# Kernel optimization log

Measured on AMD Instinct MI355X. Metric: run time of the kernel, lower is better.

The kernel has to match this reference:

```python
import jax, jax.numpy as jnp
from jax import lax
import numpy as np
import math

# --- static config (matches init_kwargs) ---
B, L, C_IN = 64, 1024, 16
D, H, D_FF = 256, 8, 1024
HS, E_LAYERS, OUT = 256, 2, 1
MA, FACTOR = 25, 3
TOP_K = int(FACTOR * math.log(L))  # 20


def _ln(x, g, b, eps=1e-5):
    m = x.mean(-1, keepdims=True)
    v = ((x - m) ** 2).mean(-1, keepdims=True)
    return (x - m) / jnp.sqrt(v + eps) * g + b


def _series_decomp(x, k):
    # x: [B, L, C]; replicate-pad then moving average (AvgPool1d stride 1)
    pad = (k - 1) // 2
    front = jnp.repeat(x[:, :1, :], pad, axis=1)
    end = jnp.repeat(x[:, -1:, :], pad, axis=1)
    xp = jnp.concatenate([front, x, end], axis=1)  # [B, L+k-1, C]
    cs = jnp.cumsum(xp, axis=1)
    cs = jnp.concatenate([jnp.zeros_like(cs[:, :1]), cs], axis=1)
    mm = (cs[:, k:] - cs[:, :-k]) / k  # [B, L, C]
    return x - mm, mm


def _autocorrelation(q, k, v):
    # q,k,v: [B, L, H, E] -> eval-mode Autoformer AutoCorrelation
    Bq, Lq, Hq, Eq = q.shape
    qf = jnp.fft.rfft(q.transpose(0, 2, 3, 1), axis=-1)  # [B,H,E,F]
    kf = jnp.fft.rfft(k.transpose(0, 2, 3, 1), axis=-1)
    corr = jnp.fft.irfft(qf * jnp.conj(kf), n=Lq, axis=-1)  # [B,H,E,L]
    mean_value = corr.mean(axis=(1, 2))  # [B, L]
    weights, delay = lax.top_k(mean_value, TOP_K)  # [B, K]
    tmp_corr = jax.nn.softmax(weights, axis=-1)
    vals = v.transpose(0, 2, 3, 1)  # [B,H,E,L]
    init = jnp.arange(Lq)

    def step(acc, dw):
        d, w = dw  # d: [B] int, w: [B] float
        idx = (init[None, :] + d[:, None]) % Lq  # circular delayed gather == roll
        pat = jnp.take_along_axis(vals, idx[:, None, None, :], axis=-1)
        return acc + pat * w[:, None, None, None], None

    agg, _ = lax.scan(step, jnp.zeros_like(vals), (delay.T, tmp_corr.T))
    return agg.transpose(0, 3, 1, 2)  # [B, L, H, E]


def _forward(x_enc, conv1_w, conv1_b, conv2_w, conv2_b, cnn_ln_g, cnn_ln_b,
             proj_w, proj_b, proj_ln_g, proj_ln_b,
             Wq, bq, Wk, bk, Wv, bv, Wo, bo, Wff1, Wff2,
             rp1_w, rp1_b, rp_ln_g, rp_ln_b, rp2_w, rp2_b):
    Bb = x_enc.shape[0]
    dn = ('NCH', 'OIH', 'NCH')
    # CNN frontend (dropout = identity in eval)
    h = lax.conv_general_dilated(x_enc.transpose(0, 2, 1), conv1_w, (1,), [(1, 1)],
                                 dimension_numbers=dn) + conv1_b[None, :, None]
    h = jax.nn.relu(h)
    h = lax.conv_general_dilated(h, conv2_w, (1,), [(1, 1)],
                                 dimension_numbers=dn) + conv2_b[None, :, None]
    h = jax.nn.relu(h)
    enc = _ln(h.transpose(0, 2, 1), cnn_ln_g, cnn_ln_b)  # [B, L, D]

    pooled_parts = []
    for i in range(E_LAYERS):
        q = (enc @ Wq[i] + bq[i]).reshape(Bb, L, H, D // H)
        k = (enc @ Wk[i] + bk[i]).reshape(Bb, L, H, D // H)
        v = (enc @ Wv[i] + bv[i]).reshape(Bb, L, H, D // H)
        ac = _autocorrelation(q, k, v).reshape(Bb, L, D)
        new_x = ac @ Wo[i] + bo[i]
        x = enc + new_x
        x, _ = _series_decomp(x, MA)
        y = jax.nn.gelu(jnp.einsum('bld,fd->blf', x, Wff1[i]), approximate=False)
        y = jnp.einsum('blf,df->bld', y, Wff2[i])
        enc, _ = _series_decomp(x + y, MA)
        pooled_parts.append(enc[:, -1, :])

    pooled = jnp.concatenate(pooled_parts, axis=-1)  # [B, e_layers*D]
    input_embed = _ln(jax.nn.relu(x_enc.reshape(Bb, -1) @ proj_w + proj_b),
                      proj_ln_g, proj_ln_b)  # [B, HS]
    final = jnp.concatenate([pooled, input_embed], axis=-1)
    o = jax.nn.relu(final @ rp1_w + rp1_b)
    o = _ln(o, rp_ln_g, rp_ln_b)
    o = o @ rp2_w + rp2_b  # [B, 1]
    return o.squeeze(-1)


def setup_inputs() -> dict:
    key = jax.random.key(0)
    ks = iter(jax.random.split(key, 32))

    def nrm(shape, s=0.02):
        return jax.random.normal(next(ks), shape, jnp.float32) * s

    inp = {
        'x_enc': jax.random.normal(next(ks), (B, L, C_IN), jnp.float32),
        'conv1_w': nrm((D, C_IN, 3), 0.1), 'conv1_b': jnp.zeros((D,), jnp.float32),
        'conv2_w': nrm((D, D, 3), 0.05), 'conv2_b': jnp.zeros((D,), jnp.float32),
        'cnn_ln_g': jnp.ones((D,), jnp.float32), 'cnn_ln_b': jnp.zeros((D,), jnp.float32),
        'proj_w': nrm((L * C_IN, HS)), 'proj_b': jnp.zeros((HS,), jnp.float32),
        'proj_ln_g': jnp.ones((HS,), jnp.float32), 'proj_ln_b': jnp.zeros((HS,), jnp.float32),
        'Wq': nrm((E_LAYERS, D, D)), 'bq': jnp.zeros((E_LAYERS, D), jnp.float32),
        'Wk': nrm((E_LAYERS, D, D)), 'bk': jnp.zeros((E_LAYERS, D), jnp.float32),
        'Wv': nrm((E_LAYERS, D, D)), 'bv': jnp.zeros((E_LAYERS, D), jnp.float32),
        'Wo': nrm((E_LAYERS, D, D)), 'bo': jnp.zeros((E_LAYERS, D), jnp.float32),
        'Wff1': nrm((E_LAYERS, D_FF, D)),
        'Wff2': nrm((E_LAYERS, D, D_FF)),
        'rp1_w': nrm((E_LAYERS * D + HS, HS)), 'rp1_b': jnp.zeros((HS,), jnp.float32),
        'rp_ln_g': jnp.ones((HS,), jnp.float32), 'rp_ln_b': jnp.zeros((HS,), jnp.float32),
        'rp2_w': nrm((HS, OUT)), 'rp2_b': jnp.zeros((OUT,), jnp.float32),
    }
    return inp


def reference(x_enc, conv1_w, conv1_b, conv2_w, conv2_b, cnn_ln_g, cnn_ln_b,
              proj_w, proj_b, proj_ln_g, proj_ln_b,
              Wq, bq, Wk, bk, Wv, bv, Wo, bo, Wff1, Wff2,
              rp1_w, rp1_b, rp_ln_g, rp_ln_b, rp2_w, rp2_b):
    return _forward(x_enc, conv1_w, conv1_b, conv2_w, conv2_b, cnn_ln_g, cnn_ln_b,
                    proj_w, proj_b, proj_ln_g, proj_ln_b,
                    Wq, bq, Wk, bk, Wv, bv, Wo, bo, Wff1, Wff2,
                    rp1_w, rp1_b, rp_ln_g, rp_ln_b, rp2_w, rp2_b)
```

## Files before the change

### kernel.cpp

```cpp
#include <hip/hip_runtime.h>
#include <math.h>

#define FLAG_ACC     1
#define FLAG_RELU    2
#define FLAG_GELU    4
#define FLAG_ABF16   8
#define FLAG_OBF16  16
#define FLAG_RESB16 32

typedef __attribute__((ext_vector_type(8))) short short8;
typedef __attribute__((ext_vector_type(4))) short short4v;
typedef __attribute__((ext_vector_type(4))) float f32x4;

__device__ __forceinline__ short f2bf(float f) {
  unsigned u = __builtin_bit_cast(unsigned, f);
  unsigned r = u + 0x7fffu + ((u >> 16) & 1u);
  return (short)(r >> 16);
}
__device__ __forceinline__ float bf2f(short s) {
  unsigned u = ((unsigned)(unsigned short)s) << 16;
  return __builtin_bit_cast(float, u);
}
__device__ __forceinline__ void load_lds16(const void* g, void* lds) {
  __builtin_amdgcn_global_load_lds(
      (const __attribute__((address_space(1))) void*)g,
      (__attribute__((address_space(3))) void*)lds, 16, 0, 0);
}

__global__ __launch_bounds__(256) void gemm_f32(
    const float* __restrict__ A, const float* __restrict__ B, float* __restrict__ C,
    int M, int N, int K, int a_shift,
    const float* __restrict__ bias, const float* __restrict__ residual, int flags)
{
  __shared__ float As[16][65];
  __shared__ float Bs[16][64];
  const int tid = threadIdx.x;
  const int tx = tid & 15, ty = tid >> 4;
  const int row0 = blockIdx.y * 64;
  const int col0 = blockIdx.x * 64;
  int kbeg = 0, kend = K;
  if ((int)gridDim.z > 1) {
    int kchunk = ((K + (int)gridDim.z - 1) / (int)gridDim.z + 15) & ~15;
    kbeg = (int)blockIdx.z * kchunk;
    kend = min(K, kbeg + kchunk);
  }
  float acc[4][4] = {};
  const int a_m = tid >> 2;
  const int a_k = (tid & 3) << 2;
  const int b_n = (tid & 15) << 2;
  const int b_k = tid >> 4;
  for (int k0 = kbeg; k0 < kend; k0 += 16) {
    int srow = row0 + a_m + a_shift;
    float4 av = make_float4(0.f, 0.f, 0.f, 0.f);
    if (srow >= 0 && srow < M)
      av = *reinterpret_cast<const float4*>(A + (long long)srow * K + (k0 + a_k));
    As[a_k + 0][a_m] = av.x; As[a_k + 1][a_m] = av.y;
    As[a_k + 2][a_m] = av.z; As[a_k + 3][a_m] = av.w;
    float4 bv = make_float4(0.f, 0.f, 0.f, 0.f);
    int brow = k0 + b_k;
    if (brow < K)
      bv = *reinterpret_cast<const float4*>(B + (long long)brow * N + (col0 + b_n));
    Bs[b_k][b_n + 0] = bv.x; Bs[b_k][b_n + 1] = bv.y;
    Bs[b_k][b_n + 2] = bv.z; Bs[b_k][b_n + 3] = bv.w;
    __syncthreads();
#pragma unroll
    for (int kk = 0; kk < 16; kk++) {
      float ar[4], br[4];
#pragma unroll
      for (int i = 0; i < 4; i++) ar[i] = As[kk][ty * 4 + i];
#pragma unroll
      for (int j = 0; j < 4; j++) br[j] = Bs[kk][tx * 4 + j];
#pragma unroll
      for (int i = 0; i < 4; i++)
#pragma unroll
        for (int j = 0; j < 4; j++)
          acc[i][j] += ar[i] * br[j];
    }
    __syncthreads();
  }
  if ((int)gridDim.z > 1) {
#pragma unroll
    for (int i = 0; i < 4; i++) {
      int r = row0 + ty * 4 + i; if (r >= M) continue;
#pragma unroll
      for (int j = 0; j < 4; j++) {
        int c = col0 + tx * 4 + j; if (c >= N) continue;
        atomicAdd(&C[(long long)r * N + c], acc[i][j]);
      }
    }
    return;
  }
#pragma unroll
  for (int i = 0; i < 4; i++) {
    int r = row0 + ty * 4 + i; if (r >= M) continue;
#pragma unroll
    for (int j = 0; j < 4; j++) {
      int c = col0 + tx * 4 + j; if (c >= N) continue;
      float v = acc[i][j];
      if (bias)     v += bias[c];
      if (residual) v += residual[(long long)r * N + c];
      if (flags & FLAG_ACC)  v += C[(long long)r * N + c];
      if (flags & FLAG_RELU) v = fmaxf(v, 0.f);
      if (flags & FLAG_GELU) v = 0.5f * v * (1.f + erff(v * 0.70710678118654752f));
      C[(long long)r * N + c] = v;
    }
  }
}

__global__ __launch_bounds__(256) void gemm_bf16_bt(
    const void* __restrict__ Av, const short* __restrict__ Btb, void* __restrict__ Cv,
    const float* __restrict__ residual, const float* __restrict__ bias,
    int M, int N, int K, int lda, int flags, int tapped)
{
  __shared__ __align__(16) short Asl[2][8192];
  __shared__ __align__(16) short Bsl[2][8192];
  const int tid = threadIdx.x;
  const int row0 = blockIdx.x * 128;
  const int col0 = blockIdx.y * 128;
  const int lane = tid & 63;
  const int wave = tid >> 6;
  const int wm = (wave >> 1) * 64;
  const int wn = (wave & 1) * 64;
  const int fm = lane & 15;
  const int k8c = lane >> 4;
  const int mr = tid >> 1;
  const int mkc = (tid & 1) * 4;
  const int msw = mr & 7;
  const bool a_dma = (flags & FLAG_ABF16) && !tapped;

  short8 sv[4];

  auto stage_dma = [&](int buf, int k0) {
#pragma unroll
    for (int u = 0; u < 4; u++) {
      int p = (wave * 4 + u) * 64 + lane;
      int r = p >> 3;
      int kc = (p & 7) ^ (r & 7);
      load_lds16(Btb + (long long)(col0 + r) * K + k0 + kc * 8,
                 (char*)Bsl[buf] + (wave * 4 + u) * 1024);
      if (a_dma)
        load_lds16((const short*)Av + (long long)(row0 + r) * lda + k0 + kc * 8,
                   (char*)Asl[buf] + (wave * 4 + u) * 1024);
    }
  };
  auto loadA = [&](int k0) {
    int arow = row0 + mr + (tapped ? (k0 >> 8) - 1 : 0);
    int acol = tapped ? (k0 & 255) : k0;
    bool ok = (arow >= 0 && arow < M);
    if (flags & FLAG_ABF16) {
      const short* ga = (const short*)Av + (long long)arow * lda + acol + mkc * 8;
      short8 z;
#pragma unroll
      for (int u = 0; u < 8; u++) z[u] = 0;
#pragma unroll
      for (int j = 0; j < 4; j++) sv[j] = ok ? *(const short8*)(ga + j * 8) : z;
    } else {
      const float* ga = (const float*)Av + (long long)arow * lda + acol + mkc * 8;
#pragma unroll
      for (int j = 0; j < 4; j++) {
        float4 f0 = make_float4(0.f,0.f,0.f,0.f), f1 = f0;
        if (ok) { f0 = *(const float4*)(ga + j * 8); f1 = *(const float4*)(ga + j * 8 + 4); }
        short8 v;
        v[0]=f2bf(f0.x); v[1]=f2bf(f0.y); v[2]=f2bf(f0.z); v[3]=f2bf(f0.w);
        v[4]=f2bf(f1.x); v[5]=f2bf(f1.y); v[6]=f2bf(f1.z); v[7]=f2bf(f1.w);
        sv[j] = v;
      }
    }
  };
  auto writeA = [&](int buf) {
#pragma unroll
    for (int j = 0; j < 4; j++)
      *(short8*)&Asl[buf][(mr * 8 + ((mkc + j) ^ msw)) * 8] = sv[j];
  };

  f32x4 acc[4][4] = {};
  const int nt = K >> 6;
  stage_dma(0, 0);
  if (!a_dma) { loadA(0); writeA(0); }
  __syncthreads();
  int cur = 0;
  for (int t = 0; t < nt; t++) {
    if (t + 1 < nt) {
      stage_dma(cur ^ 1, (t + 1) << 6);
      if (!a_dma) loadA((t + 1) << 6);
    }
#pragma unroll
    for (int kk8 = 0; kk8 < 8; kk8 += 4) {
      short8 af[4], bf[4];
#pragma unroll
      for (int i = 0; i < 4; i++) {
        int r = wm + i * 16 + fm;
        af[i] = *(short8*)&Asl[cur][(r * 8 + ((kk8 + k8c) ^ (r & 7))) * 8];
      }
#pragma unroll
      for (int j = 0; j < 4; j++) {
        int r = wn + j * 16 + fm;
        bf[j] = *(short8*)&Bsl[cur][(r * 8 + ((kk8 + k8c) ^ (r & 7))) * 8];
      }
#pragma unroll
      for (int i = 0; i < 4; i++)
#pragma unroll
        for (int j = 0; j < 4; j++)
          acc[i][j] = __builtin_amdgcn_mfma_f32_16x16x32_bf16(af[i], bf[j], acc[i][j], 0, 0, 0);
    }
    if (!a_dma && t + 1 < nt) writeA(cur ^ 1);
    __syncthreads();
    cur ^= 1;
  }
#pragma unroll
  for (int i = 0; i < 4; i++) {
    const int mbase = row0 + wm + i * 16 + (lane >> 4) * 4;
#pragma unroll
    for (int j = 0; j < 4; j++) {
      const int n = col0 + wn + j * 16 + fm;
      const float bs = bias ? bias[n] : 0.f;
#pragma unroll
      for (int r = 0; r < 4; r++) {
        long long idx = (long long)(mbase + r) * N + n;
        float v = acc[i][j][r] + bs;
        if (residual) {
          if (flags & FLAG_RESB16) v += bf2f(((const short*)residual)[idx]);
          else                     v += residual[idx];
        }
        if (flags & FLAG_ACC)  v += ((const float*)Cv)[idx];
        if (flags & FLAG_RELU) v = fmaxf(v, 0.f);
        if (flags & FLAG_GELU) v = 0.5f * v * (1.f + erff(v * 0.70710678118654752f));
        if (flags & FLAG_OBF16) ((short*)Cv)[idx] = f2bf(v);
        else                    ((float*)Cv)[idx] = v;
      }
    }
  }
}

__global__ __launch_bounds__(256) void gemm_qkT(
    const short* __restrict__ Ab, const short* __restrict__ Bth,
    const short* __restrict__ Btl, float* __restrict__ QT,
    const float* __restrict__ bias, int K)
{
  __shared__ __align__(16) short Asl[2][4096];
  __shared__ __align__(16) short Bhi[2][4096];
  __shared__ __align__(16) short Blo[2][4096];
  const int tid = threadIdx.x;
  const int row0 = blockIdx.x * 128;
  const int col0 = blockIdx.y * 128;
  const int lane = tid & 63;
  const int wave = tid >> 6;
  const int wm = (wave >> 1) * 64;
  const int wn = (wave & 1) * 64;
  const int fm = lane & 15;
  const int k8c = lane >> 4;

  auto stage = [&](int buf, int k0) {
#pragma unroll
    for (int u = 0; u < 2; u++) {
      int p = (wave + u * 4) * 64 + lane;
      int r = p >> 2;
      int kc = (p & 3) ^ ((r >> 1) & 3);
      long long ao = (long long)(row0 + r) * 256 + k0 + kc * 8;
      long long go = (long long)(col0 + r) * K + k0 + kc * 8;
      int lo = (wave + u * 4) * 1024;
      load_lds16(Ab + ao, (char*)Asl[buf] + lo);
      load_lds16(Bth + go, (char*)Bhi[buf] + lo);
      load_lds16(Btl + go, (char*)Blo[buf] + lo);
    }
  };

  f32x4 acc[4][4] = {};
  const int nt = K >> 5;
  stage(0, 0);
  __syncthreads();
  int cur = 0;
  for (int t = 0; t < nt; t++) {
    if (t + 1 < nt) stage(cur ^ 1, (t + 1) << 5);
    short8 af[4], bh[4], bl[4];
#pragma unroll
    for (int i = 0; i < 4; i++) {
      int r = wm + i * 16 + fm;
      af[i] = *(short8*)&Asl[cur][(r * 4 + (k8c ^ ((r >> 1) & 3))) * 8];
    }
#pragma unroll
    for (int j = 0; j < 4; j++) {
      int r = wn + j * 16 + fm;
      int p = (r * 4 + (k8c ^ ((r >> 1) & 3))) * 8;
      bh[j] = *(short8*)&Bhi[cur][p];
      bl[j] = *(short8*)&Blo[cur][p];
    }
#pragma unroll
    for (int i = 0; i < 4; i++)
#pragma unroll
      for (int j = 0; j < 4; j++) {
        acc[i][j] = __builtin_amdgcn_mfma_f32_16x16x32_bf16(af[i], bh[j], acc[i][j], 0, 0, 0);
        acc[i][j] = __builtin_amdgcn_mfma_f32_16x16x32_bf16(af[i], bl[j], acc[i][j], 0, 0, 0);
      }
    __syncthreads();
    cur ^= 1;
  }
#pragma unroll
  for (int i = 0; i < 4; i++) {
    const int mbase = row0 + wm + i * 16 + (lane >> 4) * 4;
    const int bb = mbase >> 10;
    const int l  = mbase & 1023;
#pragma unroll
    for (int j = 0; j < 4; j++) {
      const int n = col0 + wn + j * 16 + fm;
      const float bs = bias[n];
      float4 o = make_float4(acc[i][j][0] + bs, acc[i][j][1] + bs,
                             acc[i][j][2] + bs, acc[i][j][3] + bs);
      *(float4*)&QT[((long long)(bb * 512 + n) << 10) + l] = o;
    }
  }
}

#define SKW(i) ((i) + ((i) >> 5))

__device__ __forceinline__ int rev4_10(int f) {
  return ((f & 3) << 8) | (((f >> 2) & 3) << 6) | (((f >> 4) & 3) << 4)
       | (((f >> 6) & 3) << 2) | ((f >> 8) & 3);
}

template<int M, bool INV, int NCH>
__device__ __forceinline__ void fft_stageN(float2 (*__restrict__ buf)[1056],
                                           const float2* __restrict__ tw, int t) {
  constexpr int LOG2M = (M == 256) ? 8 : (M == 64) ? 6 : (M == 16) ? 4 : (M == 4) ? 2 : 0;
  const int j = t & (M - 1);
  const int base = ((t >> LOG2M) << (LOG2M + 2)) | j;
  float2 w = tw[SKW(j << (8 - LOG2M))];
  const float c1 = w.x, s1 = INV ? -w.y : w.y;
  const float c2 = c1 * c1 - s1 * s1, s2 = 2.f * c1 * s1;
  const float c3 = c2 * c1 - s2 * s1, s3 = c2 * s1 + s2 * c1;
#pragma unroll
  for (int ch = 0; ch < NCH; ch++) {
    float2* s = buf[ch];
    float2 a0 = s[SKW(base)];
    float2 b0 = s[SKW(base + M)];
    float2 d0 = s[SKW(base + 2 * M)];
    float2 e0 = s[SKW(base + 3 * M)];
    float t0r = a0.x + d0.x, t0i = a0.y + d0.y;
    float t1r = a0.x - d0.x, t1i = a0.y - d0.y;
    float t2r = b0.x + e0.x, t2i = b0.y + e0.y;
    float t3r = b0.x - e0.x, t3i = b0.y - e0.y;
    float y0r = t0r + t2r, y0i = t0i + t2i;
    float y2r = t0r - t2r, y2i = t0i - t2i;
    float y1r, y1i, y3r, y3i;
    if (!INV) { y1r = t1r + t3i; y1i = t1i - t3r; y3r = t1r - t3i; y3i = t1i + t3r; }
    else      { y1r = t1r - t3i; y1i = t1i + t3r; y3r = t1r + t3i; y3i = t1i - t3r; }
    s[SKW(base)]         = make_float2(y0r, y0i);
    s[SKW(base + M)]     = make_float2(y1r * c1 - y1i * s1, y1r * s1 + y1i * c1);
    s[SKW(base + 2 * M)] = make_float2(y2r * c2 - y2i * s2, y2r * s2 + y2i * c2);
    s[SKW(base + 3 * M)] = make_float2(y3r * c3 - y3i * s3, y3r * s3 + y3i * c3);
  }
}

__global__ __launch_bounds__(256) void fft_cross(
    const float* __restrict__ QT, float* __restrict__ Rpart)
{
  __shared__ float2 buf[4][1056];
  __shared__ float2 tw[264];
  const int tid = threadIdx.x;
  const int b = blockIdx.x & 63;
  const int g = blockIdx.x >> 6;
  {
    float s, c;
    sincosf(-1.5707963267948966f * (float)tid * (1.f / 256.f), &s, &c);
    tw[SKW(tid)] = make_float2(c, s);
  }
  const float* Qb = QT + (long long)b * 524288;
  const int c0 = g * 16;
  float4 qv[4], kv[4];
#pragma unroll
  for (int c = 0; c < 4; c++) {
    qv[c] = *(const float4*)(Qb + ((long long)(c0 + c) << 10) + tid * 4);
    kv[c] = *(const float4*)(Qb + ((long long)(256 + c0 + c) << 10) + tid * 4);
  }
  float aR[4] = {0.f, 0.f, 0.f, 0.f}, aI[4] = {0.f, 0.f, 0.f, 0.f};
  __syncthreads();
  for (int q4 = 0; q4 < 4; q4++) {
    const int i0 = tid * 4;
#pragma unroll
    for (int c = 0; c < 4; c++) {
      buf[c][SKW(i0 + 0)] = make_float2(qv[c].x, kv[c].x);
      buf[c][SKW(i0 + 1)] = make_float2(qv[c].y, kv[c].y);
      buf[c][SKW(i0 + 2)] = make_float2(qv[c].z, kv[c].z);
      buf[c][SKW(i0 + 3)] = make_float2(qv[c].w, kv[c].w);
    }
    if (q4 < 3) {
      const int cb = c0 + (q4 + 1) * 4;
#pragma unroll
      for (int c = 0; c < 4; c++) {
        qv[c] = *(const float4*)(Qb + ((long long)(cb + c) << 10) + tid * 4);
        kv[c] = *(const float4*)(Qb + ((long long)(256 + cb + c) << 10) + tid * 4);
      }
    }
    __syncthreads();
    fft_stageN<256, false, 4>(buf, tw, tid); __syncthreads();
    fft_stageN<64,  false, 4>(buf, tw, tid); __syncthreads();
    fft_stageN<16,  false, 4>(buf, tw, tid); __syncthreads();
    fft_stageN<4,   false, 4>(buf, tw, tid); __syncthreads();
    fft_stageN<1,   false, 4>(buf, tw, tid); __syncthreads();
#pragma unroll
    for (int u = 0; u < 4; u++) {
      const int f = tid + (u << 8);
      const int p1 = SKW(rev4_10(f));
      const int p2 = SKW(rev4_10((1024 - f) & 1023));
#pragma unroll
      for (int c = 0; c < 4; c++) {
        float2 z1 = buf[c][p1];
        float2 z2 = buf[c][p2];
        float Qr = 0.5f * (z1.x + z2.x), Qi = 0.5f * (z1.y - z2.y);
        float Kr = 0.5f * (z1.y + z2.y), Ki = 0.5f * (z2.x - z1.x);
        aR[u] += Qr * Kr + Qi * Ki;
        aI[u] += Qi * Kr - Qr * Ki;
      }
    }
    __syncthreads();
  }
  float* Rp = Rpart + (long long)(g * 64 + b) * 2048;
#pragma unroll
  for (int u = 0; u < 4; u++) {
    Rp[tid + (u << 8)] = aR[u];
    Rp[1024 + tid + (u << 8)] = aI[u];
  }
}

__global__ __launch_bounds__(256) void fft_inv(
    const float* __restrict__ Rpart, float* __restrict__ MV)
{
  __shared__ float2 ping[1056], tw[264];
  const int tid = threadIdx.x;
  const int b = blockIdx.x;
  {
    float s, c;
    sincosf(-1.5707963267948966f * (float)tid * (1.f / 256.f), &s, &c);
    tw[SKW(tid)] = make_float2(c, s);
  }
#pragma unroll
  for (int u = 0; u < 4; u++) {
    int f = tid + (u << 8);
    float sr = 0.f, si = 0.f;
#pragma unroll
    for (int g = 0; g < 16; g++) {
      const float* Rp = Rpart + (long long)(g * 64 + b) * 2048;
      sr += Rp[f];
      si += Rp[1024 + f];
    }
    ping[SKW(f)] = make_float2(sr, si);
  }
  __syncthreads();
  float2 (*bp)[1056] = reinterpret_cast<float2 (*)[1056]>(ping);
  fft_stageN<256, true, 1>(bp, tw, tid); __syncthreads();
  fft_stageN<64,  true, 1>(bp, tw, tid); __syncthreads();
  fft_stageN<16,  true, 1>(bp, tw, tid); __syncthreads();
  fft_stageN<4,   true, 1>(bp, tw, tid); __syncthreads();
  fft_stageN<1,   true, 1>(bp, tw, tid); __syncthreads();
  const float sc = 1.f / (1024.f * 256.f);
#pragma unroll
  for (int u = 0; u < 4; u++) {
    int p = tid + (u << 8);
    MV[(long long)b * 1024 + rev4_10(p)] = ping[SKW(p)].x * sc;
  }
}

__global__ void prep_weights(
    const float* __restrict__ conv2_w, const float* __restrict__ Wq,
    const float* __restrict__ Wk, const float* __restrict__ Wff1,
    const float* __restrict__ Wff2,
    const float* __restrict__ bq, const float* __restrict__ bk,
    short* __restrict__ CB2Tb, short* __restrict__ QKTH, short* __restrict__ QKTL,
    short* __restrict__ WFF1b, short* __restrict__ WFF2b, float* __restrict__ BQK)
{
  const int total = 196608 + 262144 + 524288 + 524288 + 1024;
  for (int idx = blockIdx.x * 256 + threadIdx.x; idx < total;
       idx += gridDim.x * 256) {
    int t = idx;
    if (t < 196608) {
      int o = t / 768, rem = t % 768, kk = rem >> 8, i = rem & 255;
      CB2Tb[t] = f2bf(conv2_w[(o * 256 + i) * 3 + kk]);
    } else if ((t -= 196608) < 262144) {
      int L = t >> 17, rem = t & 131071, r = rem >> 8, k = rem & 255;
      float val = (r < 256) ? Wq[L * 65536 + k * 256 + r]
                            : Wk[L * 65536 + k * 256 + (r - 256)];
      short h = f2bf(val);
      QKTH[t] = h;
      QKTL[t] = f2bf(val - bf2f(h));
    } else if ((t -= 262144) < 524288) {
      WFF1b[t] = f2bf(Wff1[t]);
    } else if ((t -= 524288) < 524288) {
      WFF2b[t] = f2bf(Wff2[t]);
    } else {
      t -= 524288;
      int L = t >> 9, j = t & 511;
      BQK[t] = (j < 256) ? bq[L * 256 + j] : bk[L * 256 + (j - 256)];
    }
  }
}

__global__ void vo_finish(const float* __restrict__ WVO, const float* __restrict__ Wo,
                          const float* __restrict__ bv, const float* __restrict__ bo,
                          short* __restrict__ WVOTb, float* __restrict__ BVO)
{
  const int total = 131072 + 512;
  for (int idx = blockIdx.x * 256 + threadIdx.x; idx < total;
       idx += gridDim.x * 256) {
    if (idx < 131072) {
      int L = idx >> 16, rem = idx & 65535, n = rem >> 8, k = rem & 255;
      WVOTb[idx] = f2bf(WVO[L * 65536 + k * 256 + n]);
    } else {
      int j = idx - 131072;
      int L = j >> 8, n = j & 255;
      float acc = bo[L * 256 + n];
      for (int k = 0; k < 256; k++)
        acc += bv[L * 256 + k] * Wo[(long long)L * 65536 + k * 256 + n];
      BVO[j] = acc;
    }
  }
}

__global__ __launch_bounds__(256) void conv1_direct(
    const float* __restrict__ x, const float* __restrict__ w,
    const float* __restrict__ bias, short* __restrict__ out)
{
  __shared__ float xs[66][16];
  const int b = blockIdx.y, lg = blockIdx.x, tid = threadIdx.x;
  const int l0 = lg * 64;
  for (int idx = tid; idx < 1056; idx += 256) {
    int r = idx >> 4, c = idx & 15;
    int l = l0 + r - 1;
    xs[r][c] = (l >= 0 && l < 1024) ? x[((long long)b * 1024 + l) * 16 + c] : 0.f;
  }
  float wr[48];
#pragma unroll
  for (int u = 0; u < 48; u++) wr[u] = w[tid * 48 + u];
  const float bs = bias[tid];
  __syncthreads();
  for (int r = 0; r < 64; r++) {
    float acc = bs;
#pragma unroll
    for (int i = 0; i < 16; i++) {
      acc += xs[r + 0][i] * wr[i * 3 + 0];
      acc += xs[r + 1][i] * wr[i * 3 + 1];
      acc += xs[r + 2][i] * wr[i * 3 + 2];
    }
    out[((long long)b * 1024 + l0 + r) * 256 + tid] = f2bf(fmaxf(acc, 0.f));
  }
}

__global__ void fixup_conv_b(short* __restrict__ h, const short* __restrict__ src,
                             const float* __restrict__ w, const float* __restrict__ bias)
{
  int b = blockIdx.x >> 1;
  int l = (blockIdx.x & 1) ? 1023 : 0;
  int o = threadIdx.x;
  float acc = bias[o];
  for (int kk = 0; kk < 3; kk++) {
    int t = l + kk - 1;
    if (t < 0 || t > 1023) continue;
    const short* srow = src + ((long long)b * 1024 + t) * 256;
    const float* wrow = w + (long long)o * 256 * 3 + kk;
    for (int i = 0; i < 256; i++) acc += bf2f(srow[i]) * wrow[(long long)i * 3];
  }
  h[((long long)b * 1024 + l) * 256 + o] = f2bf(fmaxf(acc, 0.f));
}

__global__ __launch_bounds__(256) void ln_rows4(
    const float* __restrict__ in, float* __restrict__ out,
    const float* __restrict__ g, const float* __restrict__ b,
    int prerelu, int out_stride, int out_off)
{
  const int row = blockIdx.x * 4 + (threadIdx.x >> 6);
  const int lane = threadIdx.x & 63;
  float4 x = ((const float4*)(in + (long long)row * 256))[lane];
  if (prerelu) {
    x.x = fmaxf(x.x, 0.f); x.y = fmaxf(x.y, 0.f);
    x.z = fmaxf(x.z, 0.f); x.w = fmaxf(x.w, 0.f);
  }
  float s = x.x + x.y + x.z + x.w;
#pragma unroll
  for (int o = 32; o > 0; o >>= 1) s += __shfl_xor(s, o, 64);
  float mean = s * (1.f / 256.f);
  float4 d = make_float4(x.x - mean, x.y - mean, x.z - mean, x.w - mean);
  float s2 = d.x * d.x + d.y * d.y + d.z * d.z + d.w * d.w;
#pragma unroll
  for (int o = 32; o > 0; o >>= 1) s2 += __shfl_xor(s2, o, 64);
  float rsd = rsqrtf(s2 * (1.f / 256.f) + 1e-5f);
  float4 gg = ((const float4*)g)[lane];
  float4 bb = ((const float4*)b)[lane];
  float4 o4 = make_float4(d.x * rsd * gg.x + bb.x, d.y * rsd * gg.y + bb.y,
                          d.z * rsd * gg.z + bb.z, d.w * rsd * gg.w + bb.w);
  ((float4*)(out + (long long)row * out_stride + out_off))[lane] = o4;
}

__global__ __launch_bounds__(256) void ln_rows4bb(
    const short* __restrict__ in, short* __restrict__ out,
    const float* __restrict__ g, const float* __restrict__ b)
{
  const int row = blockIdx.x * 4 + (threadIdx.x >> 6);
  const int lane = threadIdx.x & 63;
  short4v xb = ((const short4v*)in)[(long long)row * 64 + lane];
  float4 x = make_float4(bf2f(xb[0]), bf2f(xb[1]), bf2f(xb[2]), bf2f(xb[3]));
  float s = x.x + x.y + x.z + x.w;
#pragma unroll
  for (int o = 32; o > 0; o >>= 1) s += __shfl_xor(s, o, 64);
  float mean = s * (1.f / 256.f);
  float4 d = make_float4(x.x - mean, x.y - mean, x.z - mean, x.w - mean);
  float s2 = d.x * d.x + d.y * d.y + d.z * d.z + d.w * d.w;
#pragma unroll
  for (int o = 32; o > 0; o >>= 1) s2 += __shfl_xor(s2, o, 64);
  float rsd = rsqrtf(s2 * (1.f / 256.f) + 1e-5f);
  float4 gg = ((const float4*)g)[lane];
  float4 bb = ((const float4*)b)[lane];
  short4v o4;
  o4[0] = f2bf(d.x * rsd * gg.x + bb.x);
  o4[1] = f2bf(d.y * rsd * gg.y + bb.y);
  o4[2] = f2bf(d.z * rsd * gg.z + bb.z);
  o4[3] = f2bf(d.w * rsd * gg.w + bb.w);
  ((short4v*)out)[(long long)row * 64 + lane] = o4;
}

__global__ void decomp4bf(const short* __restrict__ in, short* __restrict__ out,
                          float* __restrict__ fin, int finoff)
{
  const int id = blockIdx.x;
  const int c = id & 7;
  const int s = id >> 3;
  const int b = c + 8 * (s >> 8);
  const int lg = s & 255;
  const int l = lg * 4 + (threadIdx.x >> 6);
  const int c4 = threadIdx.x & 63;
  const short4v* base = (const short4v*)(in + (long long)b * 262144);
  float4 acc = make_float4(0.f, 0.f, 0.f, 0.f);
#pragma unroll
  for (int j = -12; j <= 12; j++) {
    int t = l + j;
    t = t < 0 ? 0 : (t > 1023 ? 1023 : t);
    short4v x = base[t * 64 + c4];
    acc.x += bf2f(x[0]); acc.y += bf2f(x[1]);
    acc.z += bf2f(x[2]); acc.w += bf2f(x[3]);
  }
  short4v x0 = base[l * 64 + c4];
  float4 o = make_float4(bf2f(x0[0]) - acc.x * (1.f / 25.f),
                         bf2f(x0[1]) - acc.y * (1.f / 25.f),
                         bf2f(x0[2]) - acc.z * (1.f / 25.f),
                         bf2f(x0[3]) - acc.w * (1.f / 25.f));
  short4v ob;
  ob[0] = f2bf(o.x); ob[1] = f2bf(o.y); ob[2] = f2bf(o.z); ob[3] = f2bf(o.w);
  ((short4v*)out)[((long long)b * 1024 + l) * 64 + c4] = ob;
  if (l == 1023) {
    float* f = fin + (long long)b * 768 + finoff + c4 * 4;
    f[0] = o.x; f[1] = o.y; f[2] = o.z; f[3] = o.w;
  }
}

__global__ void decomp4b(const short* __restrict__ in, short* __restrict__ out)
{
  const int id = blockIdx.x;
  const int c = id & 7;
  const int s = id >> 3;
  const int b = c + 8 * (s >> 8);
  const int lg = s & 255;
  const int l = lg * 4 + (threadIdx.x >> 6);
  const int c4 = threadIdx.x & 63;
  const short4v* base = (const short4v*)(in + (long long)b * 262144);
  float4 acc = make_float4(0.f, 0.f, 0.f, 0.f);
#pragma unroll
  for (int j = -12; j <= 12; j++) {
    int t = l + j;
    t = t < 0 ? 0 : (t > 1023 ? 1023 : t);
    short4v x = base[t * 64 + c4];
    acc.x += bf2f(x[0]); acc.y += bf2f(x[1]);
    acc.z += bf2f(x[2]); acc.w += bf2f(x[3]);
  }
  short4v x0 = base[l * 64 + c4];
  short4v o;
  o[0] = f2bf(bf2f(x0[0]) - acc.x * (1.f / 25.f));
  o[1] = f2bf(bf2f(x0[1]) - acc.y * (1.f / 25.f));
  o[2] = f2bf(bf2f(x0[2]) - acc.z * (1.f / 25.f));
  o[3] = f2bf(bf2f(x0[3]) - acc.w * (1.f / 25.f));
  ((short4v*)(out + (long long)b * 262144))[l * 64 + c4] = o;
}

__global__ __launch_bounds__(64) void topk_softmax_wave(
    const float* __restrict__ mv, float* __restrict__ wts, int* __restrict__ dly)
{
  const int b = blockIdx.x, lane = threadIdx.x;
  float v[16];
#pragma unroll
  for (int j = 0; j < 16; j++)
    v[j] = mv[(long long)b * 1024 + lane + 64 * j];
  float selv = 0.f; int seli = 0;
  for (int it = 0; it < 20; it++) {
    float bv = -1e30f; int bi = 0x7fffffff;
#pragma unroll
    for (int j = 0; j < 16; j++) {
      float x = v[j]; int idx = lane + 64 * j;
      if (x > bv || (x == bv && idx < bi)) { bv = x; bi = idx; }
    }
#pragma unroll
    for (int off = 32; off > 0; off >>= 1) {
      float ov = __shfl_xor(bv, off, 64);
      int   oi = __shfl_xor(bi, off, 64);
      if (ov > bv || (ov == bv && oi < bi)) { bv = ov; bi = oi; }
    }
    if (lane == it) { selv = bv; seli = bi; }
    if ((bi & 63) == lane) v[bi >> 6] = -1e30f;
  }
  const float w0 = __shfl(selv, 0, 64);
  float e = (lane < 20) ? __expf(selv - w0) : 0.f;
  float s = e;
#pragma unroll
  for (int off = 32; off > 0; off >>= 1) s += __shfl_xor(s, off, 64);
  if (lane < 20) {
    wts[b * 20 + lane] = e / s;
    dly[b * 20 + lane] = seli;
  }
}

__global__ void agg4b(const short* __restrict__ enc, const float* __restrict__ wts,
                      const int* __restrict__ dly, short* __restrict__ out)
{
  const int id = blockIdx.x;
  const int c = id & 7;
  const int s = id >> 3;
  const int b = c + 8 * (s >> 8);
  const int lg = s & 255;
  const int l = lg * 4 + (threadIdx.x >> 6);
  const int c4 = threadIdx.x & 63;
  const short4v* vb = (const short4v*)(enc + (long long)b * 262144);
  float4 acc = make_float4(0.f, 0.f, 0.f, 0.f);
  for (int kk = 0; kk < 20; kk++) {
    int d = dly[b * 20 + kk];
    float w = wts[b * 20 + kk];
    short4v x = vb[((l + d) & 1023) * 64 + c4];
    acc.x += w * bf2f(x[0]); acc.y += w * bf2f(x[1]);
    acc.z += w * bf2f(x[2]); acc.w += w * bf2f(x[3]);
  }
  short4v o;
  o[0] = f2bf(acc.x); o[1] = f2bf(acc.y); o[2] = f2bf(acc.z); o[3] = f2bf(acc.w);
  ((short4v*)(out + (long long)b * 262144))[l * 64 + c4] = o;
}

__global__ void init_bias(float* __restrict__ C, const float* __restrict__ bias)
{
  C[(long long)blockIdx.x * 256 + threadIdx.x] = bias[threadIdx.x];
}

__global__ void rp2_kernel(const float* __restrict__ x, const float* __restrict__ w,
                           const float* __restrict__ bias, float* __restrict__ out)
{
  __shared__ float red[4];
  int b = blockIdx.x, tid = threadIdx.x;
  float p = x[b * 256 + tid] * w[tid];
#pragma unroll
  for (int o = 32; o > 0; o >>= 1) p += __shfl_down(p, o, 64);
  if ((tid & 63) == 0) red[tid >> 6] = p;
  __syncthreads();
  if (tid == 0) out[b] = red[0] + red[1] + red[2] + red[3] + bias[0];
}

static inline void gemm(hipStream_t s, const float* A, const float* B, float* C,
                        int M, int N, int K, int shift, const float* bias,
                        const float* res, int flags, int splitz = 1)
{
  dim3 g((N + 63) / 64, (M + 63) / 64, splitz);
  gemm_f32<<<g, dim3(256), 0, s>>>(A, B, C, M, N, K, shift, bias, res, flags);
}

extern "C" void kernel_launch(void* const* d_in, const int* in_sizes, int n_in,
                              void* d_out, int out_size, void* d_ws, size_t ws_size,
                              hipStream_t stream)
{
  const float* x_enc  = (const float*)d_in[0];
  const float* conv1_w= (const float*)d_in[1];
  const float* conv1_b= (const float*)d_in[2];
  const float* conv2_w= (const float*)d_in[3];
  const float* conv2_b= (const float*)d_in[4];
  const float* cnn_g  = (const float*)d_in[5];
  const float* cnn_b  = (const float*)d_in[6];
  const float* proj_w = (const float*)d_in[7];
  const float* proj_b = (const float*)d_in[8];
  const float* pln_g  = (const float*)d_in[9];
  const float* pln_b  = (const float*)d_in[10];
  const float* Wq     = (const float*)d_in[11];
  const float* bq     = (const float*)d_in[12];
  const float* Wk     = (const float*)d_in[13];
  const float* bk     = (const float*)d_in[14];
  const float* Wv     = (const float*)d_in[15];
  const float* bv     = (const float*)d_in[16];
  const float* Wo     = (const float*)d_in[17];
  const float* bo     = (const float*)d_in[18];
  const float* Wff1   = (const float*)d_in[19];
  const float* Wff2   = (const float*)d_in[20];
  const float* rp1_w  = (const float*)d_in[21];
  const float* rp1_b  = (const float*)d_in[22];
  const float* rln_g  = (const float*)d_in[23];
  const float* rln_b  = (const float*)d_in[24];
  const float* rp2_w  = (const float*)d_in[25];
  const float* rp2_b  = (const float*)d_in[26];
  (void)in_sizes; (void)n_in;

  const size_t BLD = 64ull * 1024 * 256;
  size_t need;
  {
    size_t o = 3 * BLD
             + 98304 + 131072 + 131072 + 262144 + 262144
             + 65536 + 512 + 1024
             + 1048576 + 1280 + 1280 + 16384 + 49152 + 16384 + 16384;
    need = o * sizeof(float);
  }
  if (ws_size < need) {
    hipMemsetAsync(d_out, 0, (size_t)out_size * sizeof(float), stream);
    return;
  }

  float* ws = (float*)d_ws;
  size_t off = 0;
  auto alloc = [&](size_t n) { float* p = ws + off; off += n; return p; };
  float* BUF0 = alloc(BLD);
  float* BUF1 = alloc(BLD);
  float* BUF2 = alloc(BLD);
  short* CB2Tb = (short*)alloc(98304);
  short* QKTH  = (short*)alloc(131072);
  short* QKTL  = (short*)alloc(131072);
  short* WFF1b = (short*)alloc(262144);
  short* WFF2b = (short*)alloc(262144);
  short* WVOTb = (short*)alloc(65536);
  float* BVO  = alloc(512);
  float* BQK  = alloc(1024);
  float* MV16 = alloc(1048576);
  float* WTS  = alloc(1280);
  int*   DLY  = (int*)alloc(1280);
  float* PE   = alloc(16384);
  float* FIN  = alloc(49152);
  float* O1   = alloc(16384);
  float* O2   = alloc(16384);
  float* WVO  = BUF0;
  short* ENC  = (short*)BUF2;
  float* QT   = BUF0;
  float* RP   = BUF2 + 8388608;
  float* MV   = MV16;

  const int M = 65536;
  dim3 blk(256);

  prep_weights<<<1024, blk, 0, stream>>>(conv2_w, Wq, Wk, Wff1, Wff2, bq, bk,
                                         CB2Tb, QKTH, QKTL, WFF1b, WFF2b, BQK);
  for (int i = 0; i < 2; i++)
    gemm(stream, Wv + (size_t)i * 65536, Wo + (size_t)i * 65536,
         WVO + (size_t)i * 65536, 256, 256, 256, 0, nullptr, nullptr, 0);
  vo_finish<<<516, blk, 0, stream>>>(WVO, Wo, bv, bo, WVOTb, BVO);

  conv1_direct<<<dim3(16, 64), blk, 0, stream>>>(x_enc, conv1_w, conv1_b, (short*)BUF0);
  gemm_bf16_bt<<<dim3(512, 2), blk, 0, stream>>>(
      BUF0, CB2Tb, BUF1, nullptr, conv2_b, M, 256, 768, 256,
      FLAG_ABF16 | FLAG_RELU | FLAG_OBF16, 1);
  fixup_conv_b<<<128, blk, 0, stream>>>((short*)BUF1, (const short*)BUF0,
                                        conv2_w, conv2_b);
  ln_rows4bb<<<16384, blk, 0, stream>>>((const short*)BUF1, ENC, cnn_g, cnn_b);

  for (int i = 0; i < 2; i++) {
    gemm_qkT<<<dim3(512, 4), blk, 0, stream>>>(
        ENC, QKTH + (size_t)i * 131072, QKTL + (size_t)i * 131072,
        QT, BQK + i * 512, 256);
    fft_cross<<<dim3(1024), blk, 0, stream>>>(QT, RP);
    fft_inv<<<64, blk, 0, stream>>>(RP, MV);
    topk_softmax_wave<<<64, dim3(64), 0, stream>>>(MV, WTS, DLY);
    agg4b<<<dim3(16384), blk, 0, stream>>>(ENC, WTS, DLY, (short*)BUF0);
    gemm_bf16_bt<<<dim3(512, 2), blk, 0, stream>>>(
        BUF0, WVOTb + (size_t)i * 65536, BUF1, (const float*)ENC, BVO + i * 256,
        M, 256, 256, 256, FLAG_ABF16 | FLAG_OBF16 | FLAG_RESB16, 0);
    decomp4b<<<16384, blk, 0, stream>>>((const short*)BUF1, (short*)BUF0);
    for (int c = 0; c < 2; c++) {
      const short* xd = (const short*)BUF0 + (size_t)c * 32768 * 256;
      gemm_bf16_bt<<<dim3(256, 8), blk, 0, stream>>>(
          xd, WFF1b + (size_t)i * 262144, BUF2, nullptr, nullptr,
          32768, 1024, 256, 256, FLAG_ABF16 | FLAG_GELU | FLAG_OBF16, 0);
      gemm_bf16_bt<<<dim3(256, 2), blk, 0, stream>>>(
          BUF2, WFF2b + (size_t)i * 262144,
          (short*)BUF1 + (size_t)c * 32768 * 256,
          (const float*)xd, nullptr,
          32768, 256, 1024, 1024, FLAG_ABF16 | FLAG_RESB16 | FLAG_OBF16, 0);
    }
    decomp4bf<<<16384, blk, 0, stream>>>((const short*)BUF1, ENC, FIN, i * 256);
  }

  init_bias<<<64, blk, 0, stream>>>(PE, proj_b);
  gemm(stream, x_enc, proj_w, PE, 64, 256, 16384, 0, nullptr, nullptr, 0, 32);
  ln_rows4<<<16, blk, 0, stream>>>(PE, FIN, pln_g, pln_b, 1, 768, 512);
  init_bias<<<64, blk, 0, stream>>>(O1, rp1_b);
  gemm(stream, FIN, rp1_w, O1, 64, 256, 768, 0, nullptr, nullptr, 0, 4);
  ln_rows4<<<16, blk, 0, stream>>>(O1, O2, rln_g, rln_b, 1, 256, 0);
  rp2_kernel<<<64, blk, 0, stream>>>(O2, rp2_w, rp2_b, (float*)d_out);
}
```

Before: 1.523 ms.

## Fuse FFN up-projection, GELU and down-projection into one kernel

Replaces the two chunked FFN GEMM launches per layer with a single fused kernel. Each 64-row block keeps its input tile in LDS, computes a 128-wide slice of the hidden layer, applies GELU into LDS, and accumulates the down-projection in registers before adding the residual. This removes the round trip of the 1024-wide hidden activation through global memory. In exchange, the weight operands are read directly from global memory with no LDS staging, and there are two block barriers per hidden chunk, which may cap MFMA throughput.

```diff
diff --git a/kernel.cpp b/kernel.cpp
--- a/kernel.cpp
+++ b/kernel.cpp
@@ -227,6 +227,109 @@
         if (flags & FLAG_GELU) v = 0.5f * v * (1.f + erff(v * 0.70710678118654752f));
         if (flags & FLAG_OBF16) ((short*)Cv)[idx] = f2bf(v);
         else                    ((float*)Cv)[idx] = v;
+      }
+    }
+  }
+}
+
+__global__ __launch_bounds__(512) void ffn_fused(
+    const short* __restrict__ xd, const short* __restrict__ W1b,
+    const short* __restrict__ W2b, short* __restrict__ out)
+{
+  __shared__ __align__(16) short xs[16384];
+  __shared__ __align__(16) short ss[8192];
+  const int tid = threadIdx.x;
+  const int lane = tid & 63;
+  const int wave = tid >> 6;
+  const int rg = wave >> 2;
+  const int cg = wave & 3;
+  const int fm = lane & 15;
+  const int k8c = lane >> 4;
+  const long long r0 = (long long)blockIdx.x * 64;
+
+#pragma unroll
+  for (int ps = 0; ps < 4; ps++) {
+    int p = ps * 512 + tid;
+    int r = p >> 5;
+    int s = p & 31;
+    int c = s ^ (r & 7);
+    load_lds16(xd + (r0 + r) * 256 + c * 8, (char*)xs + p * 16);
+  }
+  f32x4 acc[2][4] = {};
+  __syncthreads();
+
+  for (int hc = 0; hc < 8; hc++) {
+    f32x4 s1[2][2] = {};
+#pragma unroll
+    for (int kt = 0; kt < 8; kt++) {
+      short8 a[2], b[2];
+#pragma unroll
+      for (int i = 0; i < 2; i++) {
+        int row = rg * 32 + i * 16 + fm;
+        int slot = (kt * 4 + k8c) ^ (row & 7);
+        a[i] = *(const short8*)&xs[row * 256 + slot * 8];
+      }
+#pragma unroll
+      for (int j = 0; j < 2; j++) {
+        int f = hc * 128 + cg * 32 + j * 16 + fm;
+        b[j] = *(const short8*)&W1b[(long long)f * 256 + kt * 32 + k8c * 8];
+      }
+#pragma unroll
+      for (int i = 0; i < 2; i++)
+#pragma unroll
+        for (int j = 0; j < 2; j++)
+          s1[i][j] = __builtin_amdgcn_mfma_f32_16x16x32_bf16(a[i], b[j], s1[i][j], 0, 0, 0);
+    }
+#pragma unroll
+    for (int i = 0; i < 2; i++) {
+      int rowb = rg * 32 + i * 16 + (lane >> 4) * 4;
+#pragma unroll
+      for (int j = 0; j < 2; j++) {
+        int col = cg * 32 + j * 16 + fm;
+#pragma unroll
+        for (int r = 0; r < 4; r++) {
+          int row = rowb + r;
+          float v = s1[i][j][r];
+          v = 0.5f * v * (1.f + erff(v * 0.70710678118654752f));
+          int slot = (col >> 3) ^ (row & 7);
+          ss[row * 128 + slot * 8 + (col & 7)] = f2bf(v);
+        }
+      }
+    }
+    __syncthreads();
+#pragma unroll
+    for (int kk = 0; kk < 4; kk++) {
+      short8 a[2], b[4];
+#pragma unroll
+      for (int i = 0; i < 2; i++) {
+        int row = rg * 32 + i * 16 + fm;
+        int slot = (kk * 4 + k8c) ^ (row & 7);
+        a[i] = *(const short8*)&ss[row * 128 + slot * 8];
+      }
+#pragma unroll
+      for (int j = 0; j < 4; j++) {
+        int n = cg * 64 + j * 16 + fm;
+        b[j] = *(const short8*)&W2b[(long long)n * 1024 + hc * 128 + kk * 32 + k8c * 8];
+      }
+#pragma unroll
+      for (int i = 0; i < 2; i++)
+#pragma unroll
+        for (int j = 0; j < 4; j++)
+          acc[i][j] = __builtin_amdgcn_mfma_f32_16x16x32_bf16(a[i], b[j], acc[i][j], 0, 0, 0);
+    }
+    __syncthreads();
+  }
+#pragma unroll
+  for (int i = 0; i < 2; i++) {
+    int rowb = rg * 32 + i * 16 + (lane >> 4) * 4;
+#pragma unroll
+    for (int j = 0; j < 4; j++) {
+      int n = cg * 64 + j * 16 + fm;
+#pragma unroll
+      for (int r = 0; r < 4; r++) {
+        int row = rowb + r;
+        float res = bf2f(xs[row * 256 + (((n >> 3) ^ (row & 7)) * 8) + (n & 7)]);
+        out[(r0 + row) * 256 + n] = f2bf(acc[i][j][r] + res);
       }
     }
   }
@@ -868,17 +971,9 @@
         BUF0, WVOTb + (size_t)i * 65536, BUF1, (const float*)ENC, BVO + i * 256,
         M, 256, 256, 256, FLAG_ABF16 | FLAG_OBF16 | FLAG_RESB16, 0);
     decomp4b<<<16384, blk, 0, stream>>>((const short*)BUF1, (short*)BUF0);
-    for (int c = 0; c < 2; c++) {
-      const short* xd = (const short*)BUF0 + (size_t)c * 32768 * 256;
-      gemm_bf16_bt<<<dim3(256, 8), blk, 0, stream>>>(
-          xd, WFF1b + (size_t)i * 262144, BUF2, nullptr, nullptr,
-          32768, 1024, 256, 256, FLAG_ABF16 | FLAG_GELU | FLAG_OBF16, 0);
-      gemm_bf16_bt<<<dim3(256, 2), blk, 0, stream>>>(
-          BUF2, WFF2b + (size_t)i * 262144,
-          (short*)BUF1 + (size_t)c * 32768 * 256,
-          (const float*)xd, nullptr,
-          32768, 256, 1024, 1024, FLAG_ABF16 | FLAG_RESB16 | FLAG_OBF16, 0);
-    }
+    ffn_fused<<<dim3(1024), dim3(512), 0, stream>>>(
+        (const short*)BUF0, WFF1b + (size_t)i * 262144,
+        WFF2b + (size_t)i * 262144, (short*)BUF1);
     decomp4bf<<<16384, blk, 0, stream>>>((const short*)BUF1, ENC, FIN, i * 256);
   }
 
```

Measured after the change: 1.637 ms. 7.5% more time.
